# Kernel optimization log

Measured on AMD Instinct MI355X. Metric: run time of the kernel, lower is better.

Reference implementation:

```python
import jax, jax.numpy as jnp
import numpy as np

TEMPERATURE = 1.0
EPS = 1e-5
COS_EPS = 1e-8  # torch CosineSimilarity default eps
N_POS, N_NEG, D = 512, 512, 512


def setup_inputs() -> dict:
    key = jax.random.key(0)
    k1, k2, k3 = jax.random.split(key, 3)
    tensor_positive = jax.random.normal(k1, (N_POS, D), dtype=jnp.float32)
    tensor_negative = jax.random.normal(k2, (N_NEG, D), dtype=jnp.float32)
    # nn.Linear(512*3, 1), weight ~ N(0, 0.02^2), bias zeros
    linear_w = jax.random.normal(k3, (1, 3 * D), dtype=jnp.float32) * 0.02
    linear_b = jnp.zeros((1,), dtype=jnp.float32)
    return {"tensor_positive": tensor_positive, "tensor_negative": tensor_negative,
            "linear_w": linear_w, "linear_b": linear_b}


def _cos_matrix(a, b):
    # pairwise cosine similarity [Na, Nb], matching torch CosineSimilarity eps clamp
    an = a / jnp.maximum(jnp.linalg.norm(a, axis=-1, keepdims=True), COS_EPS)
    bn = b / jnp.maximum(jnp.linalg.norm(b, axis=-1, keepdims=True), COS_EPS)
    return an @ bn.T


def reference(tensor_positive, tensor_negative, linear_w, linear_b):
    pos, neg = tensor_positive, tensor_negative
    n_pos, d = pos.shape
    n_neg = neg.shape[0]

    # NCE part
    logit_n = jnp.exp(_cos_matrix(pos, neg) / TEMPERATURE)        # [N, M]
    deno_n = jnp.sum(logit_n, axis=-1)                            # [N]
    logit_p = jnp.exp(_cos_matrix(pos, pos) / TEMPERATURE)        # [N, N]
    loss = jnp.sum(-jnp.log(logit_p / (deno_n[:, None] + logit_p + EPS)))

    # Pairwise classifier: linear(cat([a, b, |a-b|])) decomposed as
    # a@w1 + b@w2 + |a-b|@w3 to avoid materializing the 3D concat.
    w = linear_w[0]
    w1, w2, w3 = w[:d], w[d:2 * d], w[2 * d:]
    allv = jnp.concatenate([pos, neg], axis=0)                    # [N+M, D]
    t1 = pos @ w1                                                 # [N]
    t2 = allv @ w2                                                # [N+M]
    diff = jnp.abs(pos[:, None, :] - allv[None, :, :])            # [N, N+M, D]
    t3 = jnp.einsum('nmd,d->nm', diff, w3)                        # [N, N+M]
    logits = t1[:, None] + t2[None, :] + t3 + linear_b[0]
    labels = jnp.concatenate([jnp.ones((n_pos,), jnp.float32),
                              jnp.zeros((n_neg,), jnp.float32)])  # [N+M]
    # BCE(sigmoid(logits), labels), stable form; per-i mean then sum over i
    bce = labels[None, :] * jax.nn.softplus(-logits) + (1.0 - labels[None, :]) * jax.nn.softplus(logits)
    loss = loss + jnp.sum(jnp.mean(bce, axis=1))
    return loss
```

## Files before the change

### kernel.cpp

```cpp
#include <hip/hip_runtime.h>
#include <math.h>

#define NPOS 512
#define NNEG 512
#define DIM  512
#define NB   1024
#define EPSV 1e-5f
#define COS_EPS 1e-8f

#define WS_S_OFF 2560

__device__ __forceinline__ float softplus_f(float x) {
    return fmaxf(x, 0.f) + __logf(1.f + __expf(-fabsf(x)));
}

__global__ __launch_bounds__(256) void prep_kernel(
    const float* __restrict__ pos, const float* __restrict__ neg,
    const float* __restrict__ w, float* __restrict__ ws, float* __restrict__ out)
{
    int gtid = blockIdx.x * 256 + threadIdx.x;
    if (gtid == 0) out[0] = 0.f;
    int row  = gtid >> 6;
    int lane = threadIdx.x & 63;
    if (row >= NB) return;
    bool is_pos = row < NPOS;
    const float* r = is_pos ? pos + row * DIM : neg + (row - NPOS) * DIM;

    const float4* r4  = (const float4*)r + lane * 2;
    const float4* w14 = (const float4*)(w) + lane * 2;
    const float4* w24 = (const float4*)(w + DIM) + lane * 2;
    float4 a0 = r4[0],  a1 = r4[1];
    float4 u0 = w14[0], u1 = w14[1];
    float4 v0 = w24[0], v1 = w24[1];

    float ss  = a0.x*a0.x + a0.y*a0.y + a0.z*a0.z + a0.w*a0.w
              + a1.x*a1.x + a1.y*a1.y + a1.z*a1.z + a1.w*a1.w;
    float dw1 = a0.x*u0.x + a0.y*u0.y + a0.z*u0.z + a0.w*u0.w
              + a1.x*u1.x + a1.y*u1.y + a1.z*u1.z + a1.w*u1.w;
    float dw2 = a0.x*v0.x + a0.y*v0.y + a0.z*v0.z + a0.w*v0.w
              + a1.x*v1.x + a1.y*v1.y + a1.z*v1.z + a1.w*v1.w;

    #pragma unroll
    for (int off = 32; off; off >>= 1) {
        ss  += __shfl_xor(ss, off);
        dw1 += __shfl_xor(dw1, off);
        dw2 += __shfl_xor(dw2, off);
    }
    if (lane == 0) {
        float inv = 1.f / fmaxf(sqrtf(ss), COS_EPS);
        ws[row] = inv;
        ws[1536 + row] = dw2;
        if (is_pos) ws[1024 + row] = dw1;
    }
}

__global__ __launch_bounds__(256) void fused_kernel(
    const float* __restrict__ pos, const float* __restrict__ neg,
    const float* __restrict__ w, const float* __restrict__ lb,
    float* __restrict__ ws, float* __restrict__ out)
{
    __shared__ float As[32][36];
    __shared__ float Bs[32][36];
    __shared__ float w3s[512];
    __shared__ float wsum[4];
    float* S = ws + WS_S_OFF;

    int tid = threadIdx.x;
    int i0 = blockIdx.y * 32;
    int j0 = blockIdx.x * 32;
    const float* Asrc = pos + i0 * DIM;
    const float* Bsrc = (j0 < NPOS) ? (pos + j0 * DIM) : (neg + (j0 - NPOS) * DIM);

    if (tid < 128) *(float4*)&w3s[tid * 4] = *(const float4*)(w + 2 * DIM + tid * 4);

    int lr = tid >> 3;
    int lc = (tid & 7) * 4;
    int ti = tid >> 4;
    int tj = tid & 15;

    float c00 = 0.f, c01 = 0.f, c10 = 0.f, c11 = 0.f;
    float t00 = 0.f, t01 = 0.f, t10 = 0.f, t11 = 0.f;

    for (int k0 = 0; k0 < DIM; k0 += 32) {
        *(float4*)&As[lr][lc] = *(const float4*)(Asrc + lr * DIM + k0 + lc);
        *(float4*)&Bs[lr][lc] = *(const float4*)(Bsrc + lr * DIM + k0 + lc);
        __syncthreads();
        #pragma unroll
        for (int k = 0; k < 32; k += 4) {
            float4 a0 = *(const float4*)&As[2 * ti][k];
            float4 a1 = *(const float4*)&As[2 * ti + 1][k];
            float4 b0 = *(const float4*)&Bs[tj][k];
            float4 b1 = *(const float4*)&Bs[tj + 16][k];
            float4 wv = *(const float4*)&w3s[k0 + k];
#define STEP(cmp, wc) \
            c00 = fmaf(a0.cmp, b0.cmp, c00); \
            c01 = fmaf(a0.cmp, b1.cmp, c01); \
            c10 = fmaf(a1.cmp, b0.cmp, c10); \
            c11 = fmaf(a1.cmp, b1.cmp, c11); \
            t00 = fmaf(fabsf(a0.cmp - b0.cmp), wc, t00); \
            t01 = fmaf(fabsf(a0.cmp - b1.cmp), wc, t01); \
            t10 = fmaf(fabsf(a1.cmp - b0.cmp), wc, t10); \
            t11 = fmaf(fabsf(a1.cmp - b1.cmp), wc, t11);
            STEP(x, wv.x) STEP(y, wv.y) STEP(z, wv.z) STEP(w, wv.w)
#undef STEP
        }
        __syncthreads();
    }

    int n0 = i0 + 2 * ti, n1 = n0 + 1;
    int m0 = j0 + tj,     m1 = m0 + 16;

    float invn0 = ws[n0], invn1 = ws[n1];
    float invm0 = ws[m0], invm1 = ws[m1];
    int cm0 = (j0 < NPOS) ? m0 + NPOS : m0 - NPOS;
    int cm1 = cm0 + 16;
    S[(size_t)n0 * NB + cm0] = c00 * invn0 * invm0;
    S[(size_t)n0 * NB + cm1] = c01 * invn0 * invm1;
    S[(size_t)n1 * NB + cm0] = c10 * invn1 * invm0;
    S[(size_t)n1 * NB + cm1] = c11 * invn1 * invm1;

    float t1v0 = ws[1024 + n0], t1v1 = ws[1024 + n1];
    float t2v0 = ws[1536 + m0], t2v1 = ws[1536 + m1];
    float bias = lb[0];
    float l00 = t1v0 + t2v0 + t00 + bias;
    float l01 = t1v0 + t2v1 + t01 + bias;
    float l10 = t1v1 + t2v0 + t10 + bias;
    float l11 = t1v1 + t2v1 + t11 + bias;
    bool m_is_pos = (j0 < NPOS);
    float part;
    if (m_is_pos)
        part = softplus_f(-l00) + softplus_f(-l01) + softplus_f(-l10) + softplus_f(-l11);
    else
        part = softplus_f(l00) + softplus_f(l01) + softplus_f(l10) + softplus_f(l11);

    #pragma unroll
    for (int off = 32; off; off >>= 1) part += __shfl_xor(part, off);
    int lane = tid & 63, wave = tid >> 6;
    if (lane == 0) wsum[wave] = part;
    __syncthreads();
    if (tid == 0)
        atomicAdd(out, (wsum[0] + wsum[1] + wsum[2] + wsum[3]) * (1.f / 1024.f));
}

__global__ __launch_bounds__(256) void closs_kernel(
    const float* __restrict__ ws, float* __restrict__ out)
{
    const float* S = ws + WS_S_OFF;
    int wid  = (blockIdx.x * 256 + threadIdx.x) >> 6;
    int lane = threadIdx.x & 63;
    if (wid >= NPOS) return;
    const float* row = S + (size_t)wid * NB;

    const float4* p = (const float4*)row + lane * 2;
    float4 c0 = p[0], c1 = p[1];
    float deno = __expf(c0.x) + __expf(c0.y) + __expf(c0.z) + __expf(c0.w)
               + __expf(c1.x) + __expf(c1.y) + __expf(c1.z) + __expf(c1.w);
    #pragma unroll
    for (int off = 32; off; off >>= 1) deno += __shfl_xor(deno, off);

    const float4* q = (const float4*)(row + NNEG) + lane * 2;
    float4 d0 = q[0], d1 = q[1];
    float s = 0.f;
    s += __logf(deno + __expf(d0.x) + EPSV) - d0.x;
    s += __logf(deno + __expf(d0.y) + EPSV) - d0.y;
    s += __logf(deno + __expf(d0.z) + EPSV) - d0.z;
    s += __logf(deno + __expf(d0.w) + EPSV) - d0.w;
    s += __logf(deno + __expf(d1.x) + EPSV) - d1.x;
    s += __logf(deno + __expf(d1.y) + EPSV) - d1.y;
    s += __logf(deno + __expf(d1.z) + EPSV) - d1.z;
    s += __logf(deno + __expf(d1.w) + EPSV) - d1.w;
    #pragma unroll
    for (int off = 32; off; off >>= 1) s += __shfl_xor(s, off);
    if (lane == 0) atomicAdd(out, s);
}

extern "C" void kernel_launch(void* const* d_in, const int* in_sizes, int n_in,
                              void* d_out, int out_size, void* d_ws, size_t ws_size,
                              hipStream_t stream) {
    (void)in_sizes; (void)n_in; (void)out_size; (void)ws_size;
    const float* pos = (const float*)d_in[0];
    const float* neg = (const float*)d_in[1];
    const float* w   = (const float*)d_in[2];
    const float* lb  = (const float*)d_in[3];
    float* out = (float*)d_out;
    float* ws  = (float*)d_ws;

    prep_kernel<<<256, 256, 0, stream>>>(pos, neg, w, ws, out);
    fused_kernel<<<dim3(32, 16), 256, 0, stream>>>(pos, neg, w, lb, ws, out);
    closs_kernel<<<128, 256, 0, stream>>>(ws, out);
}
```

Before: 107.1 us.

## Use 64x64 register-blocked tiles with split-K and a fused finish kernel

Result: faster. 104.1 us (-2.9%).

```diff
diff --git a/kernel.cpp b/kernel.cpp
--- a/kernel.cpp
+++ b/kernel.cpp
@@ -2,13 +2,18 @@
 #include <math.h>
 
 #define NPOS 512
-#define NNEG 512
 #define DIM  512
 #define NB   1024
 #define EPSV 1e-5f
 #define COS_EPS 1e-8f
 
-#define WS_S_OFF 2560
+#define OFF_INV 0
+#define OFF_T1  1024
+#define OFF_T2  1536
+#define OFF_S0  2560
+#define OFF_S1  (OFF_S0 + NPOS * NB)
+#define OFF_TA  (OFF_S1 + NPOS * NB)
+#define OFF_TB  (OFF_TA + NPOS * NB)
 
 __device__ __forceinline__ float softplus_f(float x) {
     return fmaxf(x, 0.f) + __logf(1.f + __expf(-fabsf(x)));
@@ -48,130 +53,167 @@
     }
     if (lane == 0) {
         float inv = 1.f / fmaxf(sqrtf(ss), COS_EPS);
-        ws[row] = inv;
-        ws[1536 + row] = dw2;
-        if (is_pos) ws[1024 + row] = dw1;
+        ws[OFF_INV + row] = inv;
+        ws[OFF_T2 + row]  = dw2;
+        if (is_pos) ws[OFF_T1 + row] = dw1;
     }
 }
 
 __global__ __launch_bounds__(256) void fused_kernel(
     const float* __restrict__ pos, const float* __restrict__ neg,
-    const float* __restrict__ w, const float* __restrict__ lb,
-    float* __restrict__ ws, float* __restrict__ out)
+    const float* __restrict__ w, float* __restrict__ ws)
 {
-    __shared__ float As[32][36];
-    __shared__ float Bs[32][36];
-    __shared__ float w3s[512];
-    __shared__ float wsum[4];
-    float* S = ws + WS_S_OFF;
-
-    int tid = threadIdx.x;
-    int i0 = blockIdx.y * 32;
-    int j0 = blockIdx.x * 32;
-    const float* Asrc = pos + i0 * DIM;
-    const float* Bsrc = (j0 < NPOS) ? (pos + j0 * DIM) : (neg + (j0 - NPOS) * DIM);
-
-    if (tid < 128) *(float4*)&w3s[tid * 4] = *(const float4*)(w + 2 * DIM + tid * 4);
-
-    int lr = tid >> 3;
-    int lc = (tid & 7) * 4;
-    int ti = tid >> 4;
-    int tj = tid & 15;
-
-    float c00 = 0.f, c01 = 0.f, c10 = 0.f, c11 = 0.f;
-    float t00 = 0.f, t01 = 0.f, t10 = 0.f, t11 = 0.f;
-
-    for (int k0 = 0; k0 < DIM; k0 += 32) {
-        *(float4*)&As[lr][lc] = *(const float4*)(Asrc + lr * DIM + k0 + lc);
-        *(float4*)&Bs[lr][lc] = *(const float4*)(Bsrc + lr * DIM + k0 + lc);
-        __syncthreads();
+    __shared__ __align__(16) float As[64][36];
+    __shared__ __align__(16) float Bs[64][36];
+
+    const int tid = threadIdx.x;
+    const int n0 = blockIdx.y * 64;
+    const int m0 = blockIdx.x * 64;
+    const int z  = blockIdx.z;
+    const float* Asrc = pos + (size_t)n0 * DIM + z * 256;
+    const float* Bsrc = ((m0 < NPOS) ? (pos + (size_t)m0 * DIM)
+                                     : (neg + (size_t)(m0 - NPOS) * DIM)) + z * 256;
+    const float* w3 = w + 2 * DIM + z * 256;
+
+    const int lr = tid >> 3;
+    const int lc = (tid & 7) << 2;
+    const int ti = tid >> 4;
+    const int tj = tid & 15;
+
+    float c[4][4] = {{0.f}}, t[4][4] = {{0.f}};
+
+    float4 a0 = *(const float4*)(Asrc + lr * DIM + lc);
+    float4 a1 = *(const float4*)(Asrc + (lr + 32) * DIM + lc);
+    float4 b0 = *(const float4*)(Bsrc + lr * DIM + lc);
+    float4 b1 = *(const float4*)(Bsrc + (lr + 32) * DIM + lc);
+    *(float4*)&As[lr][lc]      = a0;
+    *(float4*)&As[lr + 32][lc] = a1;
+    *(float4*)&Bs[lr][lc]      = b0;
+    *(float4*)&Bs[lr + 32][lc] = b1;
+    __syncthreads();
+
+    #pragma unroll 1
+    for (int iter = 0; iter < 8; ++iter) {
+        const bool more = (iter < 7);
+        if (more) {
+            const float* ap = Asrc + (iter + 1) * 32;
+            const float* bp = Bsrc + (iter + 1) * 32;
+            a0 = *(const float4*)(ap + lr * DIM + lc);
+            a1 = *(const float4*)(ap + (lr + 32) * DIM + lc);
+            b0 = *(const float4*)(bp + lr * DIM + lc);
+            b1 = *(const float4*)(bp + (lr + 32) * DIM + lc);
+        }
+        const float* w3i = w3 + iter * 32;
         #pragma unroll
         for (int k = 0; k < 32; k += 4) {
-            float4 a0 = *(const float4*)&As[2 * ti][k];
-            float4 a1 = *(const float4*)&As[2 * ti + 1][k];
-            float4 b0 = *(const float4*)&Bs[tj][k];
-            float4 b1 = *(const float4*)&Bs[tj + 16][k];
-            float4 wv = *(const float4*)&w3s[k0 + k];
-#define STEP(cmp, wc) \
-            c00 = fmaf(a0.cmp, b0.cmp, c00); \
-            c01 = fmaf(a0.cmp, b1.cmp, c01); \
-            c10 = fmaf(a1.cmp, b0.cmp, c10); \
-            c11 = fmaf(a1.cmp, b1.cmp, c11); \
-            t00 = fmaf(fabsf(a0.cmp - b0.cmp), wc, t00); \
-            t01 = fmaf(fabsf(a0.cmp - b1.cmp), wc, t01); \
-            t10 = fmaf(fabsf(a1.cmp - b0.cmp), wc, t10); \
-            t11 = fmaf(fabsf(a1.cmp - b1.cmp), wc, t11);
-            STEP(x, wv.x) STEP(y, wv.y) STEP(z, wv.z) STEP(w, wv.w)
-#undef STEP
-        }
-        __syncthreads();
-    }
-
-    int n0 = i0 + 2 * ti, n1 = n0 + 1;
-    int m0 = j0 + tj,     m1 = m0 + 16;
-
-    float invn0 = ws[n0], invn1 = ws[n1];
-    float invm0 = ws[m0], invm1 = ws[m1];
-    int cm0 = (j0 < NPOS) ? m0 + NPOS : m0 - NPOS;
-    int cm1 = cm0 + 16;
-    S[(size_t)n0 * NB + cm0] = c00 * invn0 * invm0;
-    S[(size_t)n0 * NB + cm1] = c01 * invn0 * invm1;
-    S[(size_t)n1 * NB + cm0] = c10 * invn1 * invm0;
-    S[(size_t)n1 * NB + cm1] = c11 * invn1 * invm1;
-
-    float t1v0 = ws[1024 + n0], t1v1 = ws[1024 + n1];
-    float t2v0 = ws[1536 + m0], t2v1 = ws[1536 + m1];
-    float bias = lb[0];
-    float l00 = t1v0 + t2v0 + t00 + bias;
-    float l01 = t1v0 + t2v1 + t01 + bias;
-    float l10 = t1v1 + t2v0 + t10 + bias;
-    float l11 = t1v1 + t2v1 + t11 + bias;
-    bool m_is_pos = (j0 < NPOS);
-    float part;
-    if (m_is_pos)
-        part = softplus_f(-l00) + softplus_f(-l01) + softplus_f(-l10) + softplus_f(-l11);
-    else
-        part = softplus_f(l00) + softplus_f(l01) + softplus_f(l10) + softplus_f(l11);
+            float4 av[4], bv[4];
+            #pragma unroll
+            for (int r = 0; r < 4; ++r) av[r] = *(const float4*)&As[ti + 16 * r][k];
+            #pragma unroll
+            for (int s = 0; s < 4; ++s) bv[s] = *(const float4*)&Bs[tj + 16 * s][k];
+            const float4 wv = *(const float4*)(w3i + k);
+            #pragma unroll
+            for (int r = 0; r < 4; ++r) {
+                #pragma unroll
+                for (int s = 0; s < 4; ++s) {
+                    c[r][s] = fmaf(av[r].x, bv[s].x, c[r][s]);
+                    c[r][s] = fmaf(av[r].y, bv[s].y, c[r][s]);
+                    c[r][s] = fmaf(av[r].z, bv[s].z, c[r][s]);
+                    c[r][s] = fmaf(av[r].w, bv[s].w, c[r][s]);
+                    t[r][s] = fmaf(fabsf(av[r].x - bv[s].x), wv.x, t[r][s]);
+                    t[r][s] = fmaf(fabsf(av[r].y - bv[s].y), wv.y, t[r][s]);
+                    t[r][s] = fmaf(fabsf(av[r].z - bv[s].z), wv.z, t[r][s]);
+                    t[r][s] = fmaf(fabsf(av[r].w - bv[s].w), wv.w, t[r][s]);
+                }
+            }
+        }
+        if (more) {
+            __syncthreads();
+            *(float4*)&As[lr][lc]      = a0;
+            *(float4*)&As[lr + 32][lc] = a1;
+            *(float4*)&Bs[lr][lc]      = b0;
+            *(float4*)&Bs[lr + 32][lc] = b1;
+            __syncthreads();
+        }
+    }
+
+    float* Sp = ws + (z ? OFF_S1 : OFF_S0);
+    float* Tp = ws + (z ? OFF_TB : OFF_TA);
+    #pragma unroll
+    for (int r = 0; r < 4; ++r) {
+        int n = n0 + ti + 16 * r;
+        #pragma unroll
+        for (int s = 0; s < 4; ++s) {
+            int m = m0 + tj + 16 * s;
+            Sp[(size_t)n * NB + m] = c[r][s];
+            Tp[(size_t)n * NB + m] = t[r][s];
+        }
+    }
+}
+
+__global__ __launch_bounds__(256) void finish_kernel(
+    const float* __restrict__ lb, float* __restrict__ ws, float* __restrict__ out)
+{
+    const int n = blockIdx.x * 4 + (threadIdx.x >> 6);
+    const int l = threadIdx.x & 63;
+    const float4* S0 = (const float4*)(ws + OFF_S0 + (size_t)n * NB);
+    const float4* S1 = (const float4*)(ws + OFF_S1 + (size_t)n * NB);
+    const float4* T0 = (const float4*)(ws + OFF_TA + (size_t)n * NB);
+    const float4* T1 = (const float4*)(ws + OFF_TB + (size_t)n * NB);
+    const float invn = ws[OFF_INV + n];
+    const float t1n  = ws[OFF_T1 + n];
+    const float bias = lb[0];
+
+    float4 cj[4];
+    float eneg = 0.f;
+    #pragma unroll
+    for (int j = 0; j < 4; ++j) {
+        int i4 = l + 64 * j;
+        float4 s0 = S0[i4], s1 = S1[i4];
+        float4 inv4 = *(const float4*)(ws + OFF_INV + 4 * i4);
+        float4 cc;
+        cc.x = (s0.x + s1.x) * invn * inv4.x;
+        cc.y = (s0.y + s1.y) * invn * inv4.y;
+        cc.z = (s0.z + s1.z) * invn * inv4.z;
+        cc.w = (s0.w + s1.w) * invn * inv4.w;
+        cj[j] = cc;
+        if (j >= 2)
+            eneg += __expf(cc.x) + __expf(cc.y) + __expf(cc.z) + __expf(cc.w);
+    }
+    #pragma unroll
+    for (int off = 32; off; off >>= 1) eneg += __shfl_xor(eneg, off);
+
+    float part = 0.f;
+    #pragma unroll
+    for (int j = 0; j < 2; ++j) {
+        float4 cc = cj[j];
+        part += __logf(eneg + __expf(cc.x) + EPSV) - cc.x;
+        part += __logf(eneg + __expf(cc.y) + EPSV) - cc.y;
+        part += __logf(eneg + __expf(cc.z) + EPSV) - cc.z;
+        part += __logf(eneg + __expf(cc.w) + EPSV) - cc.w;
+    }
+
+    float bce = 0.f;
+    #pragma unroll
+    for (int j = 0; j < 4; ++j) {
+        int i4 = l + 64 * j;
+        float4 t0 = T0[i4], t1 = T1[i4];
+        float4 t2 = *(const float4*)(ws + OFF_T2 + 4 * i4);
+        float4 lg;
+        lg.x = t1n + t2.x + t0.x + t1.x + bias;
+        lg.y = t1n + t2.y + t0.y + t1.y + bias;
+        lg.z = t1n + t2.z + t0.z + t1.z + bias;
+        lg.w = t1n + t2.w + t0.w + t1.w + bias;
+        if (j < 2)
+            bce += softplus_f(-lg.x) + softplus_f(-lg.y) + softplus_f(-lg.z) + softplus_f(-lg.w);
+        else
+            bce += softplus_f(lg.x) + softplus_f(lg.y) + softplus_f(lg.z) + softplus_f(lg.w);
+    }
+    part += bce * (1.f / 1024.f);
 
     #pragma unroll
     for (int off = 32; off; off >>= 1) part += __shfl_xor(part, off);
-    int lane = tid & 63, wave = tid >> 6;
-    if (lane == 0) wsum[wave] = part;
-    __syncthreads();
-    if (tid == 0)
-        atomicAdd(out, (wsum[0] + wsum[1] + wsum[2] + wsum[3]) * (1.f / 1024.f));
-}
-
-__global__ __launch_bounds__(256) void closs_kernel(
-    const float* __restrict__ ws, float* __restrict__ out)
-{
-    const float* S = ws + WS_S_OFF;
-    int wid  = (blockIdx.x * 256 + threadIdx.x) >> 6;
-    int lane = threadIdx.x & 63;
-    if (wid >= NPOS) return;
-    const float* row = S + (size_t)wid * NB;
-
-    const float4* p = (const float4*)row + lane * 2;
-    float4 c0 = p[0], c1 = p[1];
-    float deno = __expf(c0.x) + __expf(c0.y) + __expf(c0.z) + __expf(c0.w)
-               + __expf(c1.x) + __expf(c1.y) + __expf(c1.z) + __expf(c1.w);
-    #pragma unroll
-    for (int off = 32; off; off >>= 1) deno += __shfl_xor(deno, off);
-
-    const float4* q = (const float4*)(row + NNEG) + lane * 2;
-    float4 d0 = q[0], d1 = q[1];
-    float s = 0.f;
-    s += __logf(deno + __expf(d0.x) + EPSV) - d0.x;
-    s += __logf(deno + __expf(d0.y) + EPSV) - d0.y;
-    s += __logf(deno + __expf(d0.z) + EPSV) - d0.z;
-    s += __logf(deno + __expf(d0.w) + EPSV) - d0.w;
-    s += __logf(deno + __expf(d1.x) + EPSV) - d1.x;
-    s += __logf(deno + __expf(d1.y) + EPSV) - d1.y;
-    s += __logf(deno + __expf(d1.z) + EPSV) - d1.z;
-    s += __logf(deno + __expf(d1.w) + EPSV) - d1.w;
-    #pragma unroll
-    for (int off = 32; off; off >>= 1) s += __shfl_xor(s, off);
-    if (lane == 0) atomicAdd(out, s);
+    if (l == 0) atomicAdd(out, part);
 }
 
 extern "C" void kernel_launch(void* const* d_in, const int* in_sizes, int n_in,
@@ -186,6 +228,6 @@
     float* ws  = (float*)d_ws;
 
     prep_kernel<<<256, 256, 0, stream>>>(pos, neg, w, ws, out);
-    fused_kernel<<<dim3(32, 16), 256, 0, stream>>>(pos, neg, w, lb, ws, out);
-    closs_kernel<<<128, 256, 0, stream>>>(ws, out);
-}
+    fused_kernel<<<dim3(16, 8, 2), 256, 0, stream>>>(pos, neg, w, ws);
+    finish_kernel<<<128, 256, 0, stream>>>(lb, ws, out);
+}
```
